# Kernel optimization log

Hardware: AMD Instinct MI355X
Metric: run time of the kernel (lower is better)

Reference implementation:

```python
import jax, jax.numpy as jnp
import numpy as np

# FARNN_S_D_W (RE2NN-SEQ), farnn=1, train_mode='sum' (real semiring -> plain matmul),
# additional_nonlinear='tanh', sigmoid_exponent=1, no CRF.
VOCAB, D, R, RW, S, C = 30000, 100, 150, 50, 50, 20
B, L = 256, 512


def setup_inputs() -> dict:
    key = jax.random.key(0)
    ks = jax.random.split(key, 18)
    f = lambda k, shp, s=0.1: (jax.random.normal(k, shp, dtype=jnp.float32) * s)
    return dict(
        tokens=jax.random.randint(ks[0], (B, L), 0, VOCAB),
        W_embed=f(ks[1], (VOCAB, D), 1.0),        # pretrained word embeddings
        embed_r=f(ks[2], (D, R)),                  # embed_r_generalized
        V_embed=f(ks[3], (VOCAB, R)),
        C_embed=f(ks[4], (C, R)),
        S1=f(ks[5], (S, R)),
        S2=f(ks[6], (S, R)),
        S1_w=f(ks[7], (S, RW)),
        S2_w=f(ks[8], (S, RW)),
        C_w=f(ks[9], (C, RW)),                     # C_wildcard
        WW=f(ks[10], (S, S)),                      # wildcard_wildcard
        h0=f(ks[11], (S,), 1.0),
        hT=f(ks[12], (S,), 1.0),
        beta_vec=jnp.full((R,), 0.5, jnp.float32),
        Wss1=f(ks[13], (S, S)),
        Wrs1=f(ks[14], (R, S)),
        bs1=jnp.full((1, S), 0.1, jnp.float32),
        prio_a=jnp.ones((C,), jnp.float32),        # PriorityLayer per-class scale
        prio_b=jnp.zeros((C,), jnp.float32),       # PriorityLayer per-class bias
    )


def reference(tokens, W_embed, embed_r, V_embed, C_embed, S1, S2, S1_w, S2_w,
              C_w, WW, h0, hT, beta_vec, Wss1, Wrs1, bs1, prio_a, prio_b):
    # precomputed class-summed vectors used for the hidden recurrence
    C_vec_sum = C_embed.sum(0)                                  # [R]
    Cw_sum = C_w.sum(0)                                         # [RW]
    # wildcard transition matrix: CP-recomposed wildcard + wildcard_wildcard
    wild_mat = jnp.einsum('sr,r,tr->st', S1_w, Cw_sum, S2_w) + WW  # [S,S]
    # readout vectors (hT contracted with S2 factors)
    u = hT @ S2                                                 # [R]
    uw = hT @ S2_w                                              # [RW]

    # generalized V embedding (blend of rule V factor and word embedding)
    emb_gen = jnp.tanh(W_embed[tokens] @ embed_r)               # [B,L,R]
    V_vec = V_embed[tokens] * beta_vec + emb_gen * (1.0 - beta_vec)  # [B,L,R]
    R_all = V_vec * C_vec_sum                                   # [B,L,R]

    h_init = jnp.broadcast_to(h0, (tokens.shape[0], h0.shape[0]))  # [B,S]

    def step(h, xs):
        v_vec, r_vec = xs                                       # [B,R] each
        # farnn==1 gate
        zt = jax.nn.sigmoid(h @ Wss1 + r_vec @ Wrs1 + bs1)      # [B,S]
        # semiring (sum) transition: CP-factored WFA step + wildcard path
        tr1 = (h @ S1) * r_vec                                  # [B,R]
        h_new = tr1 @ S2.T + h @ wild_mat                       # [B,S]
        h_next = zt * h_new + (1.0 - zt) * h
        # per-class local score at this step, then PriorityLayer affine
        sc = ((h @ S1) * v_vec * u) @ C_embed.T \
             + ((h @ S1_w) * uw) @ C_w.T                        # [B,C]
        sc = sc * prio_a + prio_b
        return h_next, sc

    xs = (jnp.swapaxes(V_vec, 0, 1), jnp.swapaxes(R_all, 0, 1))  # [L,B,R]
    _, scores = jax.lax.scan(step, h_init, xs)                   # [L,B,C]
    return jnp.swapaxes(scores, 0, 1)                            # [B,L,C]
```

## Files before the change

### kernel.cpp

```cpp
#include <hip/hip_runtime.h>
#include <hip/hip_bf16.h>

typedef __hip_bfloat16 bf16;
typedef __attribute__((ext_vector_type(8))) short short8v;
typedef __attribute__((ext_vector_type(4))) float floatx4;

#define VOCAB_ 30000
#define D_ 100
#define R_ 150
#define RW_ 50
#define S_ 50
#define C_ 20
#define B_ 256
#define L_ 512

__device__ __forceinline__ float b2f(bf16 x){ return __bfloat162float(x); }
__device__ __forceinline__ bf16  f2b(float x){ return __float2bfloat16(x); }

#define BAR() asm volatile("s_waitcnt lgkmcnt(0)\ns_barrier" ::: "memory")

__device__ __forceinline__ float qxor1(float x){
  return __int_as_float(
      __builtin_amdgcn_mov_dpp(__float_as_int(x), 0xB1, 0xF, 0xF, true));
}
__device__ __forceinline__ float qxor2(float x){
  return __int_as_float(
      __builtin_amdgcn_mov_dpp(__float_as_int(x), 0x4E, 0xF, 0xF, true));
}

__device__ __forceinline__ float ftanh(float x){
  const float e = __expf(2.f * x);
  return 1.f - 2.f * __builtin_amdgcn_rcpf(e + 1.f);
}

__device__ __forceinline__ float ldin(const void* p, long i, int isb){
  return isb ? b2f(((const bf16*)p)[i]) : ((const float*)p)[i];
}
template<int SB> __device__ __forceinline__ float4 ld4s(const void* p, long i4){
  if (SB) {
    uint2 r = *(const uint2*)((const unsigned short*)p + i4*4);
    float4 v;
    v.x = __uint_as_float((r.x & 0xffffu) << 16);
    v.y = __uint_as_float((r.x >> 16) << 16);
    v.z = __uint_as_float((r.y & 0xffffu) << 16);
    v.w = __uint_as_float((r.y >> 16) << 16);
    return v;
  } else {
    return ((const float4*)p)[i4];
  }
}

#define WS_WF   4096
#define WS_S2F  20480
#define WS_SW   28672
#define WS_HC   36864
#define WS_WT   53248
#define WS_ERB  139264
#define WS_ERBL 149504
#define WS_WRB  159744
#define WS_WRBL 164864
#define WS_HDR  786432

__global__ void k_pre1(const void* beta, const void* S2, const void* S2w,
                       const void* Ce, const void* Cw, const void* hT,
                       float* __restrict__ wsf)
{
  __shared__ float hTs[S_];
  __shared__ int sflag;
  int tid = threadIdx.x;
  if (tid == 0) {
    unsigned w = *(const unsigned*)beta;
    int f = (w == 0x3F003F00u) ? 1 : 0;
    sflag = f;
    ((int*)wsf)[3000] = f;
  }
  __syncthreads();
  const int isb = sflag;
  if (tid < S_) hTs[tid] = ldin(hT, tid, isb);
  __syncthreads();
  if (tid < R_) {
    float a = 0.f, c = 0.f;
    for (int s = 0; s < S_; ++s) a += hTs[s] * ldin(S2, s*R_ + tid, isb);
    for (int cc = 0; cc < C_; ++cc) c += ldin(Ce, cc*R_ + tid, isb);
    wsf[tid] = a;
    wsf[224 + tid] = c;
  }
  if (tid >= 192 && tid < 242) {
    int rw = tid - 192;
    float a = 0.f, c = 0.f;
    for (int s = 0; s < S_; ++s) a += hTs[s] * ldin(S2w, s*RW_ + rw, isb);
    for (int cc = 0; cc < C_; ++cc) c += ldin(Cw, cc*RW_ + rw, isb);
    wsf[160 + rw]  = a;
    wsf[2900 + rw] = c;
  }
}

__global__ void k_pre2(const void* S1, const void* S1w, const void* Wss1,
                       const void* WW, const void* S2, const void* S2w,
                       const void* Ce, const void* Cw, const void* er,
                       const void* Wrs1, float* __restrict__ wsf)
{
  const int isb = ((const int*)wsf)[3000];
  const int tid = threadIdx.x, blk = blockIdx.x;
  if (blk < 50) {
    const int s = blk;
    __shared__ float s2w[RW_*RW_];
    __shared__ float s1wc[RW_];
    for (int i = tid; i < RW_*RW_; i += 256) s2w[i] = ldin(S2w, i, isb);
    if (tid < RW_) s1wc[tid] = ldin(S1w, s*RW_ + tid, isb) * wsf[2900 + tid];
    __syncthreads();
    for (int col = tid; col < 300; col += 256) {
      float v;
      if (col < 150)       v = ldin(S1, s*R_ + col, isb);
      else if (col < 200)  v = ldin(S1w, s*RW_ + (col-150), isb);
      else if (col < 250)  v = ldin(Wss1, s*S_ + (col-200), isb);
      else {
        const int t2 = col - 250;
        float a = ldin(WW, s*S_ + t2, isb);
        for (int rw = 0; rw < RW_; ++rw) a += s1wc[rw] * s2w[t2*RW_ + rw];
        v = a;
      }
      wsf[WS_WF + col*52 + s] = v;
    }
    if (blk == 0) {
      for (int col = tid; col < 300; col += 256) {
        wsf[WS_WF + col*52 + 50] = 0.f;
        wsf[WS_WF + col*52 + 51] = 0.f;
      }
    }
    for (int r = tid; r < 160; r += 256)
      wsf[WS_S2F + s*160 + r] = (r < R_) ? ldin(S2, s*R_ + r, isb) : 0.f;
  } else if (blk < 64) {
    for (int c = blk - 50; c < C_; c += 14) {
      for (int k = tid; k < 224; k += 256) {
        float v = 0.f;
        if (k < R_)        v = ldin(Ce, c*R_ + k, isb);
        else if (k < 200)  v = wsf[160 + (k - R_)] * ldin(Cw, c*RW_ + (k - R_), isb);
        wsf[WS_SW + c*224 + k] = v;
      }
    }
  } else if (blk < 128) {
  } else if (blk < 138) {
    const int nt = blk - 128;
    bf16* ebh = (bf16*)(wsf + WS_ERB);
    bf16* ebl = (bf16*)(wsf + WS_ERBL);
    for (int i = tid; i < 2048; i += 256) {
      const int kk = i >> 9, lane = (i >> 3) & 63, j = i & 7;
      const int col = nt*16 + (lane & 15);
      const int k   = kk*32 + (lane >> 4)*8 + j;
      const float v = (col < R_ && k < D_) ? ldin(er, (long)k*R_ + col, isb) : 0.f;
      const bf16 h = f2b(v);
      ebh[((nt*4 + kk)*64 + lane)*8 + j] = h;
      ebl[((nt*4 + kk)*64 + lane)*8 + j] = f2b(v - b2f(h));
    }
  } else if (blk < 158) {
    const int idx = blk - 138, nt2 = idx / 5, kk = idx - nt2*5;
    bf16* wbh = (bf16*)(wsf + WS_WRB);
    bf16* wbl = (bf16*)(wsf + WS_WRBL);
    for (int i = tid; i < 512; i += 256) {
      const int lane = i >> 3, j = i & 7;
      const int s = nt2*16 + (lane & 15);
      const int k = kk*32 + (lane >> 4)*8 + j;
      const float v = (s < S_ && k < R_) ? ldin(Wrs1, (long)k*S_ + s, isb) : 0.f;
      const bf16 h = f2b(v);
      wbh[((nt2*5 + kk)*64 + lane)*8 + j] = h;
      wbl[((nt2*5 + kk)*64 + lane)*8 + j] = f2b(v - b2f(h));
    }
  }
}

__global__ void k_pre3(const void* pa, const void* pb, float* __restrict__ wsf)
{
  const int isb = ((const int*)wsf)[3000];
  const int tid = threadIdx.x;
  float* w = wsf + WS_WT + tid*96;
  for (int i = 0; i < 96; ++i) w[i] = 0.f;
  if (tid < 300) {
    for (int s = 0; s < 52; ++s) w[s] = wsf[WS_WF + tid*52 + s];
    if (tid < 150) { w[52] = wsf[224 + tid]; w[53] = wsf[tid]; }
    if (tid < 200) {
      const int s = tid >> 2, kc = tid & 3;
      for (int j = 0; j < 40; ++j)
        w[56 + j] = wsf[WS_S2F + s*160 + kc*40 + j];
    }
  } else if (tid >= 320 && tid < 400) {
    const int q = tid - 320, c = q >> 2, kc = q & 3;
    for (int j = 0; j < 56; ++j) w[j] = wsf[WS_SW + c*224 + kc*56 + j];
    w[56] = ldin(pa, c, isb);
    w[57] = ldin(pb, c, isb);
  }
}

__global__ __launch_bounds__(256)
void k_front_m32(const int* __restrict__ tokens, const void* Wembv,
                 const void* Vembv, const void* betav, const void* bs1v,
                 const float* __restrict__ wsf,
                 void* __restrict__ Voutv, void* __restrict__ Goutv,
                 int t0, int Lc)
{
  const float* Wemb = (const float*)Wembv;
  const float* Vemb = (const float*)Vembv;
  const float* beta = (const float*)betav;
  const float* bs1  = (const float*)bs1v;
  float* Vout = (float*)Voutv;
  float* Gout = (float*)Goutv;

  __shared__ __align__(16) char smem[49152];
  __shared__ int ldsTok[64];
  const int tid = threadIdx.x;
  const int lane = tid & 63, mt = tid >> 6;
  const int l15 = lane & 15, g = lane >> 4;
  const long rowbase = (long)blockIdx.x * 64;

  if (tid < 64) {
    long row = rowbase + tid;
    long b = row / Lc, l = row - b * Lc;
    ldsTok[tid] = tokens[b * L_ + t0 + l];
  }
  for (int i = tid; i < 640; i += 256) {
    const int row = i / 10, k = 150 + (i - (i/10)*10);
    const int off = row*384 + (((k >> 3) ^ (row & 7)) * 16) + (k & 7) * 2;
    *(unsigned short*)(smem + off) = 0;
    *(unsigned short*)(smem + 24576 + off) = 0;
  }
  __syncthreads();

  const int arow = mt*16 + l15;
  short8v afh[4], afl[4];
  {
    const float* wr = Wemb + (long)ldsTok[arow] * D_;
    #pragma unroll
    for (int kk = 0; kk < 4; ++kk) {
      const int k0 = kk*32 + g*8;
      float4 x0 = {0.f,0.f,0.f,0.f}, x1 = {0.f,0.f,0.f,0.f};
      if (k0 < D_)     x0 = *(const float4*)(wr + k0);
      if (k0 + 4 < D_) x1 = *(const float4*)(wr + k0 + 4);
      float xs[8] = {x0.x,x0.y,x0.z,x0.w,x1.x,x1.y,x1.z,x1.w};
      #pragma unroll
      for (int j = 0; j < 8; ++j) {
        const bf16 h = f2b(xs[j]);
        ((bf16*)&afh[kk])[j] = h;
        ((bf16*)&afl[kk])[j] = f2b(xs[j] - b2f(h));
      }
    }
  }

  const short8v* ebh = (const short8v*)(wsf + WS_ERB);
  const short8v* ebl = (const short8v*)(wsf + WS_ERBL);
  const floatx4 zero4 = {0.f, 0.f, 0.f, 0.f};
  floatx4 acc[10];
  #pragma unroll
  for (int nt = 0; nt < 10; ++nt) acc[nt] = zero4;
  #pragma unroll
  for (int nt = 0; nt < 10; ++nt) {
    #pragma unroll
    for (int kk = 0; kk < 4; ++kk) {
      const short8v bh = ebh[(nt*4 + kk)*64 + lane];
      const short8v bl = ebl[(nt*4 + kk)*64 + lane];
      acc[nt] = __builtin_amdgcn_mfma_f32_16x16x32_bf16(afh[kk], bh, acc[nt], 0,0,0);
      acc[nt] = __builtin_amdgcn_mfma_f32_16x16x32_bf16(afh[kk], bl, acc[nt], 0,0,0);
      acc[nt] = __builtin_amdgcn_mfma_f32_16x16x32_bf16(afl[kk], bh, acc[nt], 0,0,0);
    }
  }

  int rows[4]; long tb[4];
  #pragma unroll
  for (int i = 0; i < 4; ++i) {
    rows[i] = mt*16 + g*4 + i;
    tb[i] = (long)ldsTok[rows[i]] * R_;
  }
  #pragma unroll
  for (int nt = 0; nt < 10; ++nt) {
    const int r = nt*16 + l15;
    if (r < R_) {
      const float bet = beta[r];
      const float cs  = wsf[224 + r];
      const float ub  = 1.f - bet;
      #pragma unroll
      for (int i = 0; i < 4; ++i) {
        const float emb = ftanh(acc[nt][i]);
        const float vv  = Vemb[tb[i] + r];
        const float V   = vv * bet + emb * ub;
        Vout[(rowbase + rows[i]) * R_ + r] = V;
        const float vp = V * cs;
        const bf16 h = f2b(vp);
        const int off = rows[i]*384 + (((r >> 3) ^ (rows[i] & 7)) * 16) + (r & 7) * 2;
        *(bf16*)(smem + off) = h;
        *(bf16*)(smem + 24576 + off) = f2b(vp - b2f(h));
      }
    }
  }
  __syncthreads();

  short8v vfh[5], vfl[5];
  #pragma unroll
  for (int kk = 0; kk < 5; ++kk) {
    const int q2 = kk*4 + g;
    const int off = arow*384 + ((q2 ^ (arow & 7)) * 16);
    vfh[kk] = *(const short8v*)(smem + off);
    vfl[kk] = *(const short8v*)(smem + 24576 + off);
  }
  const short8v* wbh = (const short8v*)(wsf + WS_WRB);
  const short8v* wbl = (const short8v*)(wsf + WS_WRBL);
  floatx4 acc2[4];
  #pragma unroll
  for (int nt2 = 0; nt2 < 4; ++nt2) acc2[nt2] = zero4;
  #pragma unroll
  for (int nt2 = 0; nt2 < 4; ++nt2) {
    #pragma unroll
    for (int kk = 0; kk < 5; ++kk) {
      const short8v bh = wbh[(nt2*5 + kk)*64 + lane];
      const short8v bl = wbl[(nt2*5 + kk)*64 + lane];
      acc2[nt2] = __builtin_amdgcn_mfma_f32_16x16x32_bf16(vfh[kk], bh, acc2[nt2], 0,0,0);
      acc2[nt2] = __builtin_amdgcn_mfma_f32_16x16x32_bf16(vfh[kk], bl, acc2[nt2], 0,0,0);
      acc2[nt2] = __builtin_amdgcn_mfma_f32_16x16x32_bf16(vfl[kk], bh, acc2[nt2], 0,0,0);
    }
  }
  #pragma unroll
  for (int nt2 = 0; nt2 < 4; ++nt2) {
    const int s = nt2*16 + l15;
    if (s < S_) {
      const float bias = bs1[s];
      #pragma unroll
      for (int i = 0; i < 4; ++i)
        Gout[(rowbase + rows[i]) * S_ + s] = acc2[nt2][i] + bias;
    }
  }
}

__global__ __launch_bounds__(256)
void k_front_mfma(const int* __restrict__ tokens, const void* Wemb,
                  const void* Vemb, const void* beta, const void* bs1,
                  const float* __restrict__ wsf,
                  void* __restrict__ Vout, void* __restrict__ Gout,
                  int t0, int Lc)
{
  __shared__ __align__(16) char smem[45056];
  __shared__ int ldsTok[64];
  const int tid = threadIdx.x;
  const int lane = tid & 63, mt = tid >> 6;
  const int l15 = lane & 15, l4 = lane >> 4;
  const long rowbase = (long)blockIdx.x * 64;

  if (tid < 64) {
    long row = rowbase + tid;
    long b = row / Lc, l = row - b * Lc;
    ldsTok[tid] = tokens[b * L_ + t0 + l];
  }
  __syncthreads();

  for (int i4 = tid; i4 < 1024; i4 += 256) {
    const int row = i4 >> 4, q = i4 & 15;
    const unsigned short* wr = (const unsigned short*)Wemb + (long)ldsTok[row] * D_;
    uint2 lo = {0u, 0u}, hi = {0u, 0u};
    if (q < 12)       { lo = *(const uint2*)(wr + q*8); hi = *(const uint2*)(wr + q*8 + 4); }
    else if (q == 12) { lo = *(const uint2*)(wr + 96); }
    char* dst = smem + row*256 + ((q ^ (row & 7)) * 16);
    *(uint2*)dst = lo;
    *(uint2*)(dst + 8) = hi;
  }
  for (int i = tid; i < 1536; i += 256) {
    uint2 z = {0u, 0u};
    *(uint2*)(smem + 20480 + i*16) = z;
    *(uint2*)(smem + 20480 + i*16 + 8) = z;
  }
  __syncthreads();

  const int arow = mt*16 + l15;
  short8v af[4];
  #pragma unroll
  for (int kk = 0; kk < 4; ++kk)
    af[kk] = *(const short8v*)(smem + arow*256 + (((kk*4 + l4) ^ (arow & 7)) * 16));
  __syncthreads();

  const short8v* erb = (const short8v*)(wsf + WS_ERB);
  floatx4 zero4 = {0.f, 0.f, 0.f, 0.f};
  floatx4 acc[10];
  #pragma unroll
  for (int nt = 0; nt < 10; ++nt) acc[nt] = zero4;
  #pragma unroll
  for (int nt = 0; nt < 10; ++nt)
    #pragma unroll
    for (int kk = 0; kk < 4; ++kk)
      acc[nt] = __builtin_amdgcn_mfma_f32_16x16x32_bf16(
                    af[kk], erb[(nt*4 + kk)*64 + lane], acc[nt], 0, 0, 0);

  bf16* ldsVo = (bf16*)smem;
  int rows[4]; long tb[4];
  #pragma unroll
  for (int i = 0; i < 4; ++i) {
    rows[i] = mt*16 + l4*4 + i;
    tb[i] = (long)ldsTok[rows[i]] * R_;
  }
  const bf16* vem  = (const bf16*)Vemb;
  const bf16* betp = (const bf16*)beta;
  #pragma unroll
  for (int nt = 0; nt < 10; ++nt) {
    const int r = nt*16 + l15;
    if (r < R_) {
      const float bet = b2f(betp[r]);
      const float cs  = wsf[224 + r];
      const float ub  = 1.f - bet;
      #pragma unroll
      for (int i = 0; i < 4; ++i) {
        const float emb = ftanh(acc[nt][i]);
        const float vv  = b2f(vem[tb[i] + r]);
        const float V   = vv * bet + emb * ub;
        ldsVo[rows[i]*160 + r] = f2b(V);
        const int p = (r >> 3) ^ (rows[i] & 7);
        *(bf16*)(smem + 20480 + rows[i]*384 + p*16 + (r & 7)*2) = f2b(V * cs);
      }
    }
  }
  __syncthreads();

  short8v vf[5];
  #pragma unroll
  for (int kk = 0; kk < 5; ++kk)
    vf[kk] = *(const short8v*)(smem + 20480 + arow*384 + (((kk*4 + l4) ^ (arow & 7)) * 16));
  const short8v* wrb = (const short8v*)(wsf + WS_WRB);
  floatx4 acc2[4];
  #pragma unroll
  for (int nt2 = 0; nt2 < 4; ++nt2) acc2[nt2] = zero4;
  #pragma unroll
  for (int nt2 = 0; nt2 < 4; ++nt2)
    #pragma unroll
    for (int kk = 0; kk < 5; ++kk)
      acc2[nt2] = __builtin_amdgcn_mfma_f32_16x16x32_bf16(
                      vf[kk], wrb[(nt2*5 + kk)*64 + lane], acc2[nt2], 0, 0, 0);

  bf16* goutp = (bf16*)Gout;
  const bf16* bsp = (const bf16*)bs1;
  #pragma unroll
  for (int nt2 = 0; nt2 < 4; ++nt2) {
    const int s = nt2*16 + l15;
    if (s < S_) {
      const float bias = b2f(bsp[s]);
      #pragma unroll
      for (int i = 0; i < 4; ++i)
        goutp[(rowbase + rows[i]) * S_ + s] = f2b(acc2[nt2][i] + bias);
    }
  }
  const unsigned short* vo = (const unsigned short*)smem;
  unsigned short* vout = (unsigned short*)Vout;
  for (int i = tid; i < 4800; i += 256) {
    const int row = i / 75, q2 = i - row*75;
    const unsigned w = *(const unsigned*)(vo + row*160 + q2*2);
    *(unsigned*)(vout + (size_t)(rowbase + row)*R_ + q2*2) = w;
  }
}

template<int SB>
__global__ __launch_bounds__(448) __attribute__((amdgpu_waves_per_eu(2, 2)))
void k_rnn(const void* h0, float* __restrict__ wsf,
           const void* __restrict__ Vg, const void* __restrict__ Gg,
           void* __restrict__ out, int t0, int Lc)
{
  const int isb = ((const int*)wsf)[3000];
  float* hc = wsf + WS_HC;
  __shared__ __align__(16) float lds_h[56];
  __shared__ __align__(16) float tr1[160];
  __shared__ __align__(16) float BP[2][224];
  __shared__ float GP[52];
  __shared__ float HW[52];
  __shared__ __align__(16) float cV[2][1200];
  __shared__ __align__(16) float cG[2][400];
  __shared__ __align__(16) float scb[L_ * C_];
  const int tid = threadIdx.x;
  const int b = blockIdx.x;
  const size_t esz = SB ? 2 : 4;
  const char* Vsb = (const char*)Vg + (size_t)b * Lc * R_ * esz;
  const char* Gsb = (const char*)Gg + (size_t)b * Lc * S_ * esz;

  float4 W0,W1,W2,W3,W4,W5,W6,W7,W8,W9,W10,W11,W12,W13;
  float4 Q0,Q1,Q2,Q3,Q4,Q5,Q6,Q7,Q8,Q9;
  float2 PR;
  {
    const float4* wp = (const float4*)(wsf + WS_WT + tid*96);
    W0=wp[0]; W1=wp[1]; W2=wp[2]; W3=wp[3]; W4=wp[4];
    W5=wp[5]; W6=wp[6]; W7=wp[7]; W8=wp[8]; W9=wp[9];
    W10=wp[10]; W11=wp[11]; W12=wp[12]; W13=wp[13];
    Q0=wp[14]; Q1=wp[15]; Q2=wp[16]; Q3=wp[17]; Q4=wp[18];
    Q5=wp[19]; Q6=wp[20]; Q7=wp[21]; Q8=wp[22]; Q9=wp[23];
    PR = *(const float2*)(wsf + WS_WT + tid*96 + 56);
  }
  const int isP1 = (tid < 300);
  const int isP2 = (tid < 200);
  const int s0   = tid >> 2, kc2 = tid & 3;
  const int isSc = (tid >= 320 && tid < 400);
  const int qs   = isSc ? tid - 320 : 0;
  const int c0   = qs >> 2, kc3 = qs & 3;
  const int isPf = (tid < 400);
  const int qpf  = tid;

  float h_own = 0.f;
  if (isP2 && kc2 == 0)
    h_own = (t0 == 0) ? ldin(h0, s0, isb) : hc[(long)b*S_ + s0];

  if (tid < S_) lds_h[tid] = (t0 == 0) ? ldin(h0, tid, isb) : hc[(long)b*S_ + tid];
  else if (tid < 56) lds_h[tid] = 0.f;
  if (tid >= 64 && tid < 74) tr1[150 + (tid - 64)] = 0.f;
  if (tid >= 96 && tid < 120) { BP[0][200 + (tid-96)] = 0.f; BP[1][200 + (tid-96)] = 0.f; }

  float4 rS = {0,0,0,0};
  if (isPf) {
    #pragma unroll
    for (int ch = 0; ch < 2; ++ch) {
      float4 v = (qpf < 300) ? ld4s<SB>(Vsb, (long)ch*300 + qpf)
                             : ld4s<SB>(Gsb, (long)ch*100 + (qpf-300));
      if (qpf < 300) ((float4*)cV[ch])[qpf] = v;
      else           ((float4*)cG[ch])[qpf-300] = v;
    }
    rS = (qpf < 300) ? ld4s<SB>(Vsb, 2L*300 + qpf)
                     : ld4s<SB>(Gsb, 2L*100 + (qpf-300));
  }
  __syncthreads();

  for (int tb = 0; tb < Lc; tb += 8) {
    const int cb = (tb >> 3) & 1;
    const float* cVb = cV[cb];
    const float* cGb = cG[cb];
    #pragma unroll
    for (int cs = 0; cs < 8; ++cs) {
      if (isP1) {
        float a0=0.f, a1=0.f, a2=0.f, a3=0.f;
        const float4* h4 = (const float4*)lds_h;
#define P1Q(Wq, q) { const float4 hv = h4[q]; \
        a0 = fmaf(hv.x, Wq.x, a0); a1 = fmaf(hv.y, Wq.y, a1); \
        a2 = fmaf(hv.z, Wq.z, a2); a3 = fmaf(hv.w, Wq.w, a3); }
        P1Q(W0,0) P1Q(W1,1) P1Q(W2,2) P1Q(W3,3) P1Q(W4,4) P1Q(W5,5) P1Q(W6,6)
        P1Q(W7,7) P1Q(W8,8) P1Q(W9,9) P1Q(W10,10) P1Q(W11,11) P1Q(W12,12)
#undef P1Q
        const float a = (a0 + a1) + (a2 + a3);
        if (tid < 150) {
          const float v = cVb[cs*150 + tid];
          tr1[tid]        = a * (v * W13.x);
          BP[cs & 1][tid] = a * (v * W13.y);
        } else if (tid < 200) BP[cs & 1][tid] = a;
        else if (tid < 250)   GP[tid - 200] = a;
        else                  HW[tid - 250] = a;
      }
      if (isSc && (tb + cs > 0)) {
        const float4* bp4 = (const float4*)BP[(cs + 1) & 1] + kc3*14;
        float a0=0.f, a1=0.f, a2=0.f, a3=0.f;
#define SCQ(Wq, q) { const float4 tv = bp4[q]; \
        a0 = fmaf(tv.x, Wq.x, a0); a1 = fmaf(tv.y, Wq.y, a1); \
        a2 = fmaf(tv.z, Wq.z, a2); a3 = fmaf(tv.w, Wq.w, a3); }
        SCQ(W0,0) SCQ(W1,1) SCQ(W2,2) SCQ(W3,3) SCQ(W4,4) SCQ(W5,5) SCQ(W6,6)
        SCQ(W7,7) SCQ(W8,8) SCQ(W9,9) SCQ(W10,10) SCQ(W11,11) SCQ(W12,12) SCQ(W13,13)
#undef SCQ
        float a = (a0 + a1) + (a2 + a3);
        a += qxor1(a);
        a += qxor2(a);
        if (kc3 == 0) scb[(tb + cs - 1)*C_ + c0] = a * PR.x + PR.y;
      }
      if (cs == 0 && tb > 0 && isPf) {
        if (tb + 8 < Lc) {
          if (qpf < 300) ((float4*)cV[cb^1])[qpf] = rS;
          else           ((float4*)cG[cb^1])[qpf-300] = rS;
        }
        if (tb + 16 < Lc) {
          const long m = (tb + 16) >> 3;
          rS = (qpf < 300) ? ld4s<SB>(Vsb, m*300 + qpf)
                           : ld4s<SB>(Gsb, m*100 + (qpf-300));
        }
      }
      BAR();
      if (isP2) {
        float hw = 0.f, gp = 0.f, cg = 0.f;
        if (kc2 == 0) { hw = HW[s0]; gp = GP[s0]; cg = cGb[cs*50 + s0]; }
        const float4* tp4 = (const float4*)tr1 + kc2*10;
        float a0=0.f, a1=0.f, a2=0.f, a3=0.f;
#define TQ(Wq, q) { const float4 tv = tp4[q]; \
        a0 = fmaf(tv.x, Wq.x, a0); a1 = fmaf(tv.y, Wq.y, a1); \
        a2 = fmaf(tv.z, Wq.z, a2); a3 = fmaf(tv.w, Wq.w, a3); }
        TQ(Q0,0) TQ(Q1,1) TQ(Q2,2) TQ(Q3,3) TQ(Q4,4)
        TQ(Q5,5) TQ(Q6,6) TQ(Q7,7) TQ(Q8,8) TQ(Q9,9)
#undef TQ
        float a = (a0 + a1) + (a2 + a3);
        a += qxor1(a);
        a += qxor2(a);
        if (kc2 == 0) {
          const float hn = a + hw;
          const float x  = gp + cg;
          const float z  = 1.f / (1.f + __expf(-x));
          h_own = z * hn + (1.f - z) * h_own;
          lds_h[s0] = h_own;
        }
      }
      BAR();
    }
  }
  if (isSc) {
    const float4* bp4 = (const float4*)BP[(Lc - 1) & 1] + kc3*14;
    float a0=0.f, a1=0.f, a2=0.f, a3=0.f;
#define SCQ(Wq, q) { const float4 tv = bp4[q]; \
    a0 = fmaf(tv.x, Wq.x, a0); a1 = fmaf(tv.y, Wq.y, a1); \
    a2 = fmaf(tv.z, Wq.z, a2); a3 = fmaf(tv.w, Wq.w, a3); }
    SCQ(W0,0) SCQ(W1,1) SCQ(W2,2) SCQ(W3,3) SCQ(W4,4) SCQ(W5,5) SCQ(W6,6)
    SCQ(W7,7) SCQ(W8,8) SCQ(W9,9) SCQ(W10,10) SCQ(W11,11) SCQ(W12,12) SCQ(W13,13)
#undef SCQ
    float a = (a0 + a1) + (a2 + a3);
    a += qxor1(a);
    a += qxor2(a);
    if (kc3 == 0) scb[(Lc - 1)*C_ + c0] = a * PR.x + PR.y;
  }
  __syncthreads();
  {
    const long obase = (long)b * L_ * C_ + (long)t0 * C_;
    if (!isb) {
      float* op = (float*)out + obase;
      const int n4 = Lc * C_ / 4;
      for (int i = tid; i < n4; i += 448)
        ((float4*)op)[i] = ((const float4*)scb)[i];
    } else {
      bf16* op = (bf16*)out + obase;
      const int n = Lc * C_;
      for (int i = tid; i < n; i += 448) op[i] = f2b(scb[i]);
    }
  }
  if (tid < S_) hc[(long)b*S_ + tid] = lds_h[tid];
}

extern "C" void kernel_launch(void* const* d_in, const int* in_sizes, int n_in,
                              void* d_out, int out_size, void* d_ws, size_t ws_size,
                              hipStream_t stream) {
  const int*  tokens = (const int*) d_in[0];
  const void* Wemb   = d_in[1];
  const void* er     = d_in[2];
  const void* Vemb   = d_in[3];
  const void* Ce     = d_in[4];
  const void* S1     = d_in[5];
  const void* S2     = d_in[6];
  const void* S1w    = d_in[7];
  const void* S2w    = d_in[8];
  const void* Cw     = d_in[9];
  const void* WW     = d_in[10];
  const void* h0     = d_in[11];
  const void* hT     = d_in[12];
  const void* beta   = d_in[13];
  const void* Wss1   = d_in[14];
  const void* Wrs1   = d_in[15];
  const void* bs1    = d_in[16];
  const void* prioA  = d_in[17];
  const void* prioB  = d_in[18];
  float* wsf = (float*)d_ws;
  char* streamBase = (char*)d_ws + WS_HDR;

  const size_t hdr = WS_HDR;
  int sb = 0, Lc = L_;
  if (ws_size >= hdr + (size_t)B_*L_*200*4)       { sb = 0; Lc = L_; }
  else if (ws_size >= hdr + (size_t)B_*L_*200*2)  { sb = 1; Lc = L_; }
  else {
    sb = 0; Lc = 256;
    while (Lc >= 32 && hdr + (size_t)B_*Lc*200*4 > ws_size) Lc >>= 1;
    if (Lc < 32) {
      sb = 1; Lc = 256;
      while (Lc >= 32 && hdr + (size_t)B_*Lc*200*2 > ws_size) Lc >>= 1;
      if (Lc < 32) Lc = 32;
    }
  }
  const size_t esz = sb ? 2 : 4;
  void* Vbuf = (void*)streamBase;
  void* Gbuf = (void*)(streamBase + (size_t)B_ * Lc * R_ * esz);

  k_pre1<<<dim3(1), dim3(256), 0, stream>>>(beta, S2, S2w, Ce, Cw, hT, wsf);
  k_pre2<<<dim3(160), dim3(256), 0, stream>>>(S1, S1w, Wss1, WW, S2, S2w,
                                              Ce, Cw, er, Wrs1, wsf);
  k_pre3<<<dim3(1), dim3(448), 0, stream>>>(prioA, prioB, wsf);
  for (int t0 = 0; t0 < L_; t0 += Lc) {
    dim3 egrid(B_ * Lc / 64);
    if (sb) {
      k_front_mfma<<<egrid, dim3(256), 0, stream>>>(tokens, Wemb, Vemb, beta,
                                                    bs1, wsf, Vbuf, Gbuf, t0, Lc);
      k_rnn<1><<<dim3(B_), dim3(448), 0, stream>>>(h0, wsf, Vbuf, Gbuf, d_out, t0, Lc);
    } else {
      k_front_m32<<<egrid, dim3(256), 0, stream>>>(tokens, Wemb, Vemb, beta,
                                                   bs1, wsf, Vbuf, Gbuf, t0, Lc);
      k_rnn<0><<<dim3(B_), dim3(448), 0, stream>>>(h0, wsf, Vbuf, Gbuf, d_out, t0, Lc);
    }
  }
}
```

Measured before the change: 613.6 us.

## Merge precompute kernels and overlap front-end of second half with recurrence

Folds the three small precompute kernels into one multi-role launch, recomputing a few reductions locally so it needs no separate pass. Merges the front-end projection and the recurrence into one k_run kernel and splits the sequence into two halves with double buffers. The middle launch runs the recurrence for the first half and the front-end for the second half side by side, so the bandwidth-heavy front-end can hide behind the latency-bound scan. The cost is a more complex dispatch, double the intermediate buffers, and front blocks running at 448 threads with only 256 active.

```diff
diff --git a/kernel.cpp b/kernel.cpp
--- a/kernel.cpp
+++ b/kernel.cpp
@@ -54,60 +54,31 @@
 #define WS_S2F  20480
 #define WS_SW   28672
 #define WS_HC   36864
-#define WS_WT   53248
 #define WS_ERB  139264
 #define WS_ERBL 149504
 #define WS_WRB  159744
 #define WS_WRBL 164864
 #define WS_HDR  786432
 
-__global__ void k_pre1(const void* beta, const void* S2, const void* S2w,
-                       const void* Ce, const void* Cw, const void* hT,
-                       float* __restrict__ wsf)
+__global__ void k_pre(const void* beta, const void* S2, const void* S2w,
+                      const void* Ce, const void* Cw, const void* hT,
+                      const void* S1, const void* S1w, const void* Wss1,
+                      const void* WW, const void* er, const void* Wrs1,
+                      float* __restrict__ wsf)
 {
-  __shared__ float hTs[S_];
-  __shared__ int sflag;
-  int tid = threadIdx.x;
-  if (tid == 0) {
-    unsigned w = *(const unsigned*)beta;
-    int f = (w == 0x3F003F00u) ? 1 : 0;
-    sflag = f;
-    ((int*)wsf)[3000] = f;
-  }
-  __syncthreads();
-  const int isb = sflag;
-  if (tid < S_) hTs[tid] = ldin(hT, tid, isb);
-  __syncthreads();
-  if (tid < R_) {
-    float a = 0.f, c = 0.f;
-    for (int s = 0; s < S_; ++s) a += hTs[s] * ldin(S2, s*R_ + tid, isb);
-    for (int cc = 0; cc < C_; ++cc) c += ldin(Ce, cc*R_ + tid, isb);
-    wsf[tid] = a;
-    wsf[224 + tid] = c;
-  }
-  if (tid >= 192 && tid < 242) {
-    int rw = tid - 192;
-    float a = 0.f, c = 0.f;
-    for (int s = 0; s < S_; ++s) a += hTs[s] * ldin(S2w, s*RW_ + rw, isb);
-    for (int cc = 0; cc < C_; ++cc) c += ldin(Cw, cc*RW_ + rw, isb);
-    wsf[160 + rw]  = a;
-    wsf[2900 + rw] = c;
-  }
-}
-
-__global__ void k_pre2(const void* S1, const void* S1w, const void* Wss1,
-                       const void* WW, const void* S2, const void* S2w,
-                       const void* Ce, const void* Cw, const void* er,
-                       const void* Wrs1, float* __restrict__ wsf)
-{
-  const int isb = ((const int*)wsf)[3000];
   const int tid = threadIdx.x, blk = blockIdx.x;
+  const unsigned bw = *(const unsigned*)beta;
+  const int isb = (bw == 0x3F003F00u) ? 1 : 0;
   if (blk < 50) {
     const int s = blk;
     __shared__ float s2w[RW_*RW_];
     __shared__ float s1wc[RW_];
     for (int i = tid; i < RW_*RW_; i += 256) s2w[i] = ldin(S2w, i, isb);
-    if (tid < RW_) s1wc[tid] = ldin(S1w, s*RW_ + tid, isb) * wsf[2900 + tid];
+    if (tid < RW_) {
+      float c = 0.f;
+      for (int cc = 0; cc < C_; ++cc) c += ldin(Cw, cc*RW_ + tid, isb);
+      s1wc[tid] = ldin(S1w, s*RW_ + tid, isb) * c;
+    }
     __syncthreads();
     for (int col = tid; col < 300; col += 256) {
       float v;
@@ -131,17 +102,24 @@
     for (int r = tid; r < 160; r += 256)
       wsf[WS_S2F + s*160 + r] = (r < R_) ? ldin(S2, s*R_ + r, isb) : 0.f;
   } else if (blk < 64) {
+    __shared__ float uwsh[RW_];
+    if (tid < RW_) {
+      float a = 0.f;
+      for (int s = 0; s < S_; ++s)
+        a += ldin(hT, s, isb) * ldin(S2w, s*RW_ + tid, isb);
+      uwsh[tid] = a;
+    }
+    __syncthreads();
     for (int c = blk - 50; c < C_; c += 14) {
       for (int k = tid; k < 224; k += 256) {
         float v = 0.f;
         if (k < R_)        v = ldin(Ce, c*R_ + k, isb);
-        else if (k < 200)  v = wsf[160 + (k - R_)] * ldin(Cw, c*RW_ + (k - R_), isb);
+        else if (k < 200)  v = uwsh[k - R_] * ldin(Cw, c*RW_ + (k - R_), isb);
         wsf[WS_SW + c*224 + k] = v;
       }
     }
-  } else if (blk < 128) {
-  } else if (blk < 138) {
-    const int nt = blk - 128;
+  } else if (blk < 74) {
+    const int nt = blk - 64;
     bf16* ebh = (bf16*)(wsf + WS_ERB);
     bf16* ebl = (bf16*)(wsf + WS_ERBL);
     for (int i = tid; i < 2048; i += 256) {
@@ -153,8 +131,8 @@
       ebh[((nt*4 + kk)*64 + lane)*8 + j] = h;
       ebl[((nt*4 + kk)*64 + lane)*8 + j] = f2b(v - b2f(h));
     }
-  } else if (blk < 158) {
-    const int idx = blk - 138, nt2 = idx / 5, kk = idx - nt2*5;
+  } else if (blk < 94) {
+    const int idx = blk - 74, nt2 = idx / 5, kk = idx - nt2*5;
     bf16* wbh = (bf16*)(wsf + WS_WRB);
     bf16* wbl = (bf16*)(wsf + WS_WRBL);
     for (int i = tid; i < 512; i += 256) {
@@ -166,68 +144,57 @@
       wbh[((nt2*5 + kk)*64 + lane)*8 + j] = h;
       wbl[((nt2*5 + kk)*64 + lane)*8 + j] = f2b(v - b2f(h));
     }
-  }
-}
-
-__global__ void k_pre3(const void* pa, const void* pb, float* __restrict__ wsf)
+  } else {
+    if (tid == 0) ((int*)wsf)[3000] = isb;
+    if (tid < R_) {
+      float a = 0.f, c = 0.f;
+      for (int s = 0; s < S_; ++s) a += ldin(hT, s, isb) * ldin(S2, s*R_ + tid, isb);
+      for (int cc = 0; cc < C_; ++cc) c += ldin(Ce, cc*R_ + tid, isb);
+      wsf[tid] = a;
+      wsf[224 + tid] = c;
+    }
+  }
+}
+
+#define ARENA_SZ 49408
+
+__device__ void front_body(char* arena, int fblk, const int* __restrict__ tokens,
+                           const float* __restrict__ Wemb,
+                           const float* __restrict__ Vemb,
+                           const float* __restrict__ beta,
+                           const float* __restrict__ bs1,
+                           const float* __restrict__ wsf,
+                           float* __restrict__ Vout, float* __restrict__ Gout,
+                           int t0, int Lc)
 {
-  const int isb = ((const int*)wsf)[3000];
+  int* ldsTok = (int*)(arena + 49152);
   const int tid = threadIdx.x;
-  float* w = wsf + WS_WT + tid*96;
-  for (int i = 0; i < 96; ++i) w[i] = 0.f;
-  if (tid < 300) {
-    for (int s = 0; s < 52; ++s) w[s] = wsf[WS_WF + tid*52 + s];
-    if (tid < 150) { w[52] = wsf[224 + tid]; w[53] = wsf[tid]; }
-    if (tid < 200) {
-      const int s = tid >> 2, kc = tid & 3;
-      for (int j = 0; j < 40; ++j)
-        w[56 + j] = wsf[WS_S2F + s*160 + kc*40 + j];
-    }
-  } else if (tid >= 320 && tid < 400) {
-    const int q = tid - 320, c = q >> 2, kc = q & 3;
-    for (int j = 0; j < 56; ++j) w[j] = wsf[WS_SW + c*224 + kc*56 + j];
-    w[56] = ldin(pa, c, isb);
-    w[57] = ldin(pb, c, isb);
-  }
-}
-
-__global__ __launch_bounds__(256)
-void k_front_m32(const int* __restrict__ tokens, const void* Wembv,
-                 const void* Vembv, const void* betav, const void* bs1v,
-                 const float* __restrict__ wsf,
-                 void* __restrict__ Voutv, void* __restrict__ Goutv,
-                 int t0, int Lc)
-{
-  const float* Wemb = (const float*)Wembv;
-  const float* Vemb = (const float*)Vembv;
-  const float* beta = (const float*)betav;
-  const float* bs1  = (const float*)bs1v;
-  float* Vout = (float*)Voutv;
-  float* Gout = (float*)Goutv;
-
-  __shared__ __align__(16) char smem[49152];
-  __shared__ int ldsTok[64];
-  const int tid = threadIdx.x;
-  const int lane = tid & 63, mt = tid >> 6;
-  const int l15 = lane & 15, g = lane >> 4;
-  const long rowbase = (long)blockIdx.x * 64;
-
+  const long rowbase = (long)fblk * 64;
   if (tid < 64) {
     long row = rowbase + tid;
     long b = row / Lc, l = row - b * Lc;
     ldsTok[tid] = tokens[b * L_ + t0 + l];
   }
-  for (int i = tid; i < 640; i += 256) {
+  for (int i = tid; i < 640; i += 448) {
     const int row = i / 10, k = 150 + (i - (i/10)*10);
     const int off = row*384 + (((k >> 3) ^ (row & 7)) * 16) + (k & 7) * 2;
-    *(unsigned short*)(smem + off) = 0;
-    *(unsigned short*)(smem + 24576 + off) = 0;
+    *(unsigned short*)(arena + off) = 0;
+    *(unsigned short*)(arena + 24576 + off) = 0;
   }
   __syncthreads();
 
+  const int act = (tid < 256);
+  const int lane = tid & 63, mt = (tid >> 6) & 3;
+  const int l15 = lane & 15, g = lane >> 4;
   const int arow = mt*16 + l15;
+  const floatx4 zero4 = {0.f, 0.f, 0.f, 0.f};
+
   short8v afh[4], afl[4];
-  {
+  floatx4 acc[10];
+  #pragma unroll
+  for (int nt = 0; nt < 10; ++nt) acc[nt] = zero4;
+
+  if (act) {
     const float* wr = Wemb + (long)ldsTok[arow] * D_;
     #pragma unroll
     for (int kk = 0; kk < 4; ++kk) {
@@ -243,247 +210,108 @@
         ((bf16*)&afl[kk])[j] = f2b(xs[j] - b2f(h));
       }
     }
-  }
-
-  const short8v* ebh = (const short8v*)(wsf + WS_ERB);
-  const short8v* ebl = (const short8v*)(wsf + WS_ERBL);
-  const floatx4 zero4 = {0.f, 0.f, 0.f, 0.f};
-  floatx4 acc[10];
-  #pragma unroll
-  for (int nt = 0; nt < 10; ++nt) acc[nt] = zero4;
-  #pragma unroll
-  for (int nt = 0; nt < 10; ++nt) {
-    #pragma unroll
-    for (int kk = 0; kk < 4; ++kk) {
-      const short8v bh = ebh[(nt*4 + kk)*64 + lane];
-      const short8v bl = ebl[(nt*4 + kk)*64 + lane];
-      acc[nt] = __builtin_amdgcn_mfma_f32_16x16x32_bf16(afh[kk], bh, acc[nt], 0,0,0);
-      acc[nt] = __builtin_amdgcn_mfma_f32_16x16x32_bf16(afh[kk], bl, acc[nt], 0,0,0);
-      acc[nt] = __builtin_amdgcn_mfma_f32_16x16x32_bf16(afl[kk], bh, acc[nt], 0,0,0);
-    }
-  }
-
-  int rows[4]; long tb[4];
-  #pragma unroll
-  for (int i = 0; i < 4; ++i) {
-    rows[i] = mt*16 + g*4 + i;
-    tb[i] = (long)ldsTok[rows[i]] * R_;
-  }
-  #pragma unroll
-  for (int nt = 0; nt < 10; ++nt) {
-    const int r = nt*16 + l15;
-    if (r < R_) {
-      const float bet = beta[r];
-      const float cs  = wsf[224 + r];
-      const float ub  = 1.f - bet;
+    const short8v* ebh = (const short8v*)(wsf + WS_ERB);
+    const short8v* ebl = (const short8v*)(wsf + WS_ERBL);
+    #pragma unroll
+    for (int nt = 0; nt < 10; ++nt) {
       #pragma unroll
-      for (int i = 0; i < 4; ++i) {
-        const float emb = ftanh(acc[nt][i]);
-        const float vv  = Vemb[tb[i] + r];
-        const float V   = vv * bet + emb * ub;
-        Vout[(rowbase + rows[i]) * R_ + r] = V;
-        const float vp = V * cs;
-        const bf16 h = f2b(vp);
-        const int off = rows[i]*384 + (((r >> 3) ^ (rows[i] & 7)) * 16) + (r & 7) * 2;
-        *(bf16*)(smem + off) = h;
-        *(bf16*)(smem + 24576 + off) = f2b(vp - b2f(h));
+      for (int kk = 0; kk < 4; ++kk) {
+        const short8v bh = ebh[(nt*4 + kk)*64 + lane];
+        const short8v bl = ebl[(nt*4 + kk)*64 + lane];
+        acc[nt] = __builtin_amdgcn_mfma_f32_16x16x32_bf16(afh[kk], bh, acc[nt], 0,0,0);
+        acc[nt] = __builtin_amdgcn_mfma_f32_16x16x32_bf16(afh[kk], bl, acc[nt], 0,0,0);
+        acc[nt] = __builtin_amdgcn_mfma_f32_16x16x32_bf16(afl[kk], bh, acc[nt], 0,0,0);
+      }
+    }
+    int rows[4]; long tb[4];
+    #pragma unroll
+    for (int i = 0; i < 4; ++i) {
+      rows[i] = mt*16 + g*4 + i;
+      tb[i] = (long)ldsTok[rows[i]] * R_;
+    }
+    #pragma unroll
+    for (int nt = 0; nt < 10; ++nt) {
+      const int r = nt*16 + l15;
+      if (r < R_) {
+        const float bet = beta[r];
+        const float cs  = wsf[224 + r];
+        const float ub  = 1.f - bet;
+        #pragma unroll
+        for (int i = 0; i < 4; ++i) {
+          const float emb = ftanh(acc[nt][i]);
+          const float vv  = Vemb[tb[i] + r];
+          const float V   = vv * bet + emb * ub;
+          Vout[(rowbase + rows[i]) * R_ + r] = V;
+          const float vp = V * cs;
+          const bf16 h = f2b(vp);
+          const int off = rows[i]*384 + (((r >> 3) ^ (rows[i] & 7)) * 16) + (r & 7) * 2;
+          *(bf16*)(arena + off) = h;
+          *(bf16*)(arena + 24576 + off) = f2b(vp - b2f(h));
+        }
       }
     }
   }
   __syncthreads();
-
-  short8v vfh[5], vfl[5];
-  #pragma unroll
-  for (int kk = 0; kk < 5; ++kk) {
-    const int q2 = kk*4 + g;
-    const int off = arow*384 + ((q2 ^ (arow & 7)) * 16);
-    vfh[kk] = *(const short8v*)(smem + off);
-    vfl[kk] = *(const short8v*)(smem + 24576 + off);
-  }
-  const short8v* wbh = (const short8v*)(wsf + WS_WRB);
-  const short8v* wbl = (const short8v*)(wsf + WS_WRBL);
-  floatx4 acc2[4];
-  #pragma unroll
-  for (int nt2 = 0; nt2 < 4; ++nt2) acc2[nt2] = zero4;
-  #pragma unroll
-  for (int nt2 = 0; nt2 < 4; ++nt2) {
+  if (act) {
+    short8v vfh[5], vfl[5];
     #pragma unroll
     for (int kk = 0; kk < 5; ++kk) {
-      const short8v bh = wbh[(nt2*5 + kk)*64 + lane];
-      const short8v bl = wbl[(nt2*5 + kk)*64 + lane];
-      acc2[nt2] = __builtin_amdgcn_mfma_f32_16x16x32_bf16(vfh[kk], bh, acc2[nt2], 0,0,0);
-      acc2[nt2] = __builtin_amdgcn_mfma_f32_16x16x32_bf16(vfh[kk], bl, acc2[nt2], 0,0,0);
-      acc2[nt2] = __builtin_amdgcn_mfma_f32_16x16x32_bf16(vfl[kk], bh, acc2[nt2], 0,0,0);
-    }
-  }
-  #pragma unroll
-  for (int nt2 = 0; nt2 < 4; ++nt2) {
-    const int s = nt2*16 + l15;
-    if (s < S_) {
-      const float bias = bs1[s];
+      const int q2 = kk*4 + g;
+      const int off = arow*384 + ((q2 ^ (arow & 7)) * 16);
+      vfh[kk] = *(const short8v*)(arena + off);
+      vfl[kk] = *(const short8v*)(arena + 24576 + off);
+    }
+    const short8v* wbh = (const short8v*)(wsf + WS_WRB);
+    const short8v* wbl = (const short8v*)(wsf + WS_WRBL);
+    floatx4 acc2[4];
+    #pragma unroll
+    for (int nt2 = 0; nt2 < 4; ++nt2) acc2[nt2] = zero4;
+    #pragma unroll
+    for (int nt2 = 0; nt2 < 4; ++nt2) {
       #pragma unroll
-      for (int i = 0; i < 4; ++i)
-        Gout[(rowbase + rows[i]) * S_ + s] = acc2[nt2][i] + bias;
-    }
-  }
-}
-
-__global__ __launch_bounds__(256)
-void k_front_mfma(const int* __restrict__ tokens, const void* Wemb,
-                  const void* Vemb, const void* beta, const void* bs1,
-                  const float* __restrict__ wsf,
-                  void* __restrict__ Vout, void* __restrict__ Gout,
-                  int t0, int Lc)
-{
-  __shared__ __align__(16) char smem[45056];
-  __shared__ int ldsTok[64];
-  const int tid = threadIdx.x;
-  const int lane = tid & 63, mt = tid >> 6;
-  const int l15 = lane & 15, l4 = lane >> 4;
-  const long rowbase = (long)blockIdx.x * 64;
-
-  if (tid < 64) {
-    long row = rowbase + tid;
-    long b = row / Lc, l = row - b * Lc;
-    ldsTok[tid] = tokens[b * L_ + t0 + l];
-  }
-  __syncthreads();
-
-  for (int i4 = tid; i4 < 1024; i4 += 256) {
-    const int row = i4 >> 4, q = i4 & 15;
-    const unsigned short* wr = (const unsigned short*)Wemb + (long)ldsTok[row] * D_;
-    uint2 lo = {0u, 0u}, hi = {0u, 0u};
-    if (q < 12)       { lo = *(const uint2*)(wr + q*8); hi = *(const uint2*)(wr + q*8 + 4); }
-    else if (q == 12) { lo = *(const uint2*)(wr + 96); }
-    char* dst = smem + row*256 + ((q ^ (row & 7)) * 16);
-    *(uint2*)dst = lo;
-    *(uint2*)(dst + 8) = hi;
-  }
-  for (int i = tid; i < 1536; i += 256) {
-    uint2 z = {0u, 0u};
-    *(uint2*)(smem + 20480 + i*16) = z;
-    *(uint2*)(smem + 20480 + i*16 + 8) = z;
-  }
-  __syncthreads();
-
-  const int arow = mt*16 + l15;
-  short8v af[4];
-  #pragma unroll
-  for (int kk = 0; kk < 4; ++kk)
-    af[kk] = *(const short8v*)(smem + arow*256 + (((kk*4 + l4) ^ (arow & 7)) * 16));
-  __syncthreads();
-
-  const short8v* erb = (const short8v*)(wsf + WS_ERB);
-  floatx4 zero4 = {0.f, 0.f, 0.f, 0.f};
-  floatx4 acc[10];
-  #pragma unroll
-  for (int nt = 0; nt < 10; ++nt) acc[nt] = zero4;
-  #pragma unroll
-  for (int nt = 0; nt < 10; ++nt)
-    #pragma unroll
-    for (int kk = 0; kk < 4; ++kk)
-      acc[nt] = __builtin_amdgcn_mfma_f32_16x16x32_bf16(
-                    af[kk], erb[(nt*4 + kk)*64 + lane], acc[nt], 0, 0, 0);
-
-  bf16* ldsVo = (bf16*)smem;
-  int rows[4]; long tb[4];
-  #pragma unroll
-  for (int i = 0; i < 4; ++i) {
-    rows[i] = mt*16 + l4*4 + i;
-    tb[i] = (long)ldsTok[rows[i]] * R_;
-  }
-  const bf16* vem  = (const bf16*)Vemb;
-  const bf16* betp = (const bf16*)beta;
-  #pragma unroll
-  for (int nt = 0; nt < 10; ++nt) {
-    const int r = nt*16 + l15;
-    if (r < R_) {
-      const float bet = b2f(betp[r]);
-      const float cs  = wsf[224 + r];
-      const float ub  = 1.f - bet;
-      #pragma unroll
-      for (int i = 0; i < 4; ++i) {
-        const float emb = ftanh(acc[nt][i]);
-        const float vv  = b2f(vem[tb[i] + r]);
-        const float V   = vv * bet + emb * ub;
-        ldsVo[rows[i]*160 + r] = f2b(V);
-        const int p = (r >> 3) ^ (rows[i] & 7);
-        *(bf16*)(smem + 20480 + rows[i]*384 + p*16 + (r & 7)*2) = f2b(V * cs);
-      }
-    }
-  }
-  __syncthreads();
-
-  short8v vf[5];
-  #pragma unroll
-  for (int kk = 0; kk < 5; ++kk)
-    vf[kk] = *(const short8v*)(smem + 20480 + arow*384 + (((kk*4 + l4) ^ (arow & 7)) * 16));
-  const short8v* wrb = (const short8v*)(wsf + WS_WRB);
-  floatx4 acc2[4];
-  #pragma unroll
-  for (int nt2 = 0; nt2 < 4; ++nt2) acc2[nt2] = zero4;
-  #pragma unroll
-  for (int nt2 = 0; nt2 < 4; ++nt2)
-    #pragma unroll
-    for (int kk = 0; kk < 5; ++kk)
-      acc2[nt2] = __builtin_amdgcn_mfma_f32_16x16x32_bf16(
-                      vf[kk], wrb[(nt2*5 + kk)*64 + lane], acc2[nt2], 0, 0, 0);
-
-  bf16* goutp = (bf16*)Gout;
-  const bf16* bsp = (const bf16*)bs1;
-  #pragma unroll
-  for (int nt2 = 0; nt2 < 4; ++nt2) {
-    const int s = nt2*16 + l15;
-    if (s < S_) {
-      const float bias = b2f(bsp[s]);
-      #pragma unroll
-      for (int i = 0; i < 4; ++i)
-        goutp[(rowbase + rows[i]) * S_ + s] = f2b(acc2[nt2][i] + bias);
-    }
-  }
-  const unsigned short* vo = (const unsigned short*)smem;
-  unsigned short* vout = (unsigned short*)Vout;
-  for (int i = tid; i < 4800; i += 256) {
-    const int row = i / 75, q2 = i - row*75;
-    const unsigned w = *(const unsigned*)(vo + row*160 + q2*2);
-    *(unsigned*)(vout + (size_t)(rowbase + row)*R_ + q2*2) = w;
+      for (int kk = 0; kk < 5; ++kk) {
+        const short8v bh = wbh[(nt2*5 + kk)*64 + lane];
+        const short8v bl = wbl[(nt2*5 + kk)*64 + lane];
+        acc2[nt2] = __builtin_amdgcn_mfma_f32_16x16x32_bf16(vfh[kk], bh, acc2[nt2], 0,0,0);
+        acc2[nt2] = __builtin_amdgcn_mfma_f32_16x16x32_bf16(vfh[kk], bl, acc2[nt2], 0,0,0);
+        acc2[nt2] = __builtin_amdgcn_mfma_f32_16x16x32_bf16(vfl[kk], bh, acc2[nt2], 0,0,0);
+      }
+    }
+    #pragma unroll
+    for (int nt2 = 0; nt2 < 4; ++nt2) {
+      const int s = nt2*16 + l15;
+      if (s < S_) {
+        const float bias = bs1[s];
+        #pragma unroll
+        for (int i = 0; i < 4; ++i)
+          Gout[(rowbase + mt*16 + g*4 + i) * S_ + s] = acc2[nt2][i] + bias;
+      }
+    }
   }
 }
 
 template<int SB>
-__global__ __launch_bounds__(448) __attribute__((amdgpu_waves_per_eu(2, 2)))
-void k_rnn(const void* h0, float* __restrict__ wsf,
-           const void* __restrict__ Vg, const void* __restrict__ Gg,
-           void* __restrict__ out, int t0, int Lc)
+__device__ void rnn_body(char* arena, const void* h0, const void* pa,
+                         const void* pb, float* __restrict__ wsf,
+                         const void* __restrict__ Vg, const void* __restrict__ Gg,
+                         void* __restrict__ out, int t0, int Lc)
 {
   const int isb = ((const int*)wsf)[3000];
-  float* hc = wsf + WS_HC;
-  __shared__ __align__(16) float lds_h[56];
-  __shared__ __align__(16) float tr1[160];
-  __shared__ __align__(16) float BP[2][224];
-  __shared__ float GP[52];
-  __shared__ float HW[52];
-  __shared__ __align__(16) float cV[2][1200];
-  __shared__ __align__(16) float cG[2][400];
-  __shared__ __align__(16) float scb[L_ * C_];
+  float* hc    = wsf + WS_HC;
+  float* lds_h = (float*)arena;
+  float* tr1   = (float*)(arena + 224);
+  float* BPb   = (float*)(arena + 864);
+  float* GP    = (float*)(arena + 2656);
+  float* HW    = (float*)(arena + 2864);
+  float* cVb_  = (float*)(arena + 3072);
+  float* cGb_  = (float*)(arena + 12672);
+  float* scb   = (float*)(arena + 15872);
   const int tid = threadIdx.x;
   const int b = blockIdx.x;
   const size_t esz = SB ? 2 : 4;
   const char* Vsb = (const char*)Vg + (size_t)b * Lc * R_ * esz;
   const char* Gsb = (const char*)Gg + (size_t)b * Lc * S_ * esz;
 
-  float4 W0,W1,W2,W3,W4,W5,W6,W7,W8,W9,W10,W11,W12,W13;
-  float4 Q0,Q1,Q2,Q3,Q4,Q5,Q6,Q7,Q8,Q9;
-  float2 PR;
-  {
-    const float4* wp = (const float4*)(wsf + WS_WT + tid*96);
-    W0=wp[0]; W1=wp[1]; W2=wp[2]; W3=wp[3]; W4=wp[4];
-    W5=wp[5]; W6=wp[6]; W7=wp[7]; W8=wp[8]; W9=wp[9];
-    W10=wp[10]; W11=wp[11]; W12=wp[12]; W13=wp[13];
-    Q0=wp[14]; Q1=wp[15]; Q2=wp[16]; Q3=wp[17]; Q4=wp[18];
-    Q5=wp[19]; Q6=wp[20]; Q7=wp[21]; Q8=wp[22]; Q9=wp[23];
-    PR = *(const float2*)(wsf + WS_WT + tid*96 + 56);
-  }
   const int isP1 = (tid < 300);
   const int isP2 = (tid < 200);
   const int s0   = tid >> 2, kc2 = tid & 3;
@@ -493,6 +321,29 @@
   const int isPf = (tid < 400);
   const int qpf  = tid;
 
+  float4 Z4 = {0.f,0.f,0.f,0.f};
+  float4 W0=Z4,W1=Z4,W2=Z4,W3=Z4,W4=Z4,W5=Z4,W6=Z4,W7=Z4,W8=Z4,W9=Z4,
+         W10=Z4,W11=Z4,W12=Z4,W13=Z4;
+  float4 Q0=Z4,Q1=Z4,Q2=Z4,Q3=Z4,Q4=Z4,Q5=Z4,Q6=Z4,Q7=Z4,Q8=Z4,Q9=Z4;
+  float2 PR = {0.f, 0.f};
+  if (isP1) {
+    const float4* wf = (const float4*)(wsf + WS_WF + tid*52);
+    W0=wf[0]; W1=wf[1]; W2=wf[2]; W3=wf[3]; W4=wf[4]; W5=wf[5]; W6=wf[6];
+    W7=wf[7]; W8=wf[8]; W9=wf[9]; W10=wf[10]; W11=wf[11]; W12=wf[12];
+    if (tid < 150) { W13.x = wsf[224 + tid]; W13.y = wsf[tid]; }
+  } else if (isSc) {
+    const float4* sw = (const float4*)(wsf + WS_SW + c0*224 + kc3*56);
+    W0=sw[0]; W1=sw[1]; W2=sw[2]; W3=sw[3]; W4=sw[4]; W5=sw[5]; W6=sw[6];
+    W7=sw[7]; W8=sw[8]; W9=sw[9]; W10=sw[10]; W11=sw[11]; W12=sw[12]; W13=sw[13];
+    PR.x = ldin(pa, c0, isb);
+    PR.y = ldin(pb, c0, isb);
+  }
+  if (isP2) {
+    const float4* qf = (const float4*)(wsf + WS_S2F + s0*160 + kc2*40);
+    Q0=qf[0]; Q1=qf[1]; Q2=qf[2]; Q3=qf[3]; Q4=qf[4];
+    Q5=qf[5]; Q6=qf[6]; Q7=qf[7]; Q8=qf[8]; Q9=qf[9];
+  }
+
   float h_own = 0.f;
   if (isP2 && kc2 == 0)
     h_own = (t0 == 0) ? ldin(h0, s0, isb) : hc[(long)b*S_ + s0];
@@ -500,7 +351,7 @@
   if (tid < S_) lds_h[tid] = (t0 == 0) ? ldin(h0, tid, isb) : hc[(long)b*S_ + tid];
   else if (tid < 56) lds_h[tid] = 0.f;
   if (tid >= 64 && tid < 74) tr1[150 + (tid - 64)] = 0.f;
-  if (tid >= 96 && tid < 120) { BP[0][200 + (tid-96)] = 0.f; BP[1][200 + (tid-96)] = 0.f; }
+  if (tid >= 96 && tid < 120) { BPb[200 + (tid-96)] = 0.f; BPb[224 + 200 + (tid-96)] = 0.f; }
 
   float4 rS = {0,0,0,0};
   if (isPf) {
@@ -508,8 +359,8 @@
     for (int ch = 0; ch < 2; ++ch) {
       float4 v = (qpf < 300) ? ld4s<SB>(Vsb, (long)ch*300 + qpf)
                              : ld4s<SB>(Gsb, (long)ch*100 + (qpf-300));
-      if (qpf < 300) ((float4*)cV[ch])[qpf] = v;
-      else           ((float4*)cG[ch])[qpf-300] = v;
+      if (qpf < 300) ((float4*)(cVb_ + ch*1200))[qpf] = v;
+      else           ((float4*)(cGb_ + ch*400))[qpf-300] = v;
     }
     rS = (qpf < 300) ? ld4s<SB>(Vsb, 2L*300 + qpf)
                      : ld4s<SB>(Gsb, 2L*100 + (qpf-300));
@@ -518,8 +369,8 @@
 
   for (int tb = 0; tb < Lc; tb += 8) {
     const int cb = (tb >> 3) & 1;
-    const float* cVb = cV[cb];
-    const float* cGb = cG[cb];
+    const float* cVb = cVb_ + cb*1200;
+    const float* cGb = cGb_ + cb*400;
     #pragma unroll
     for (int cs = 0; cs < 8; ++cs) {
       if (isP1) {
@@ -534,14 +385,14 @@
         const float a = (a0 + a1) + (a2 + a3);
         if (tid < 150) {
           const float v = cVb[cs*150 + tid];
-          tr1[tid]        = a * (v * W13.x);
-          BP[cs & 1][tid] = a * (v * W13.y);
-        } else if (tid < 200) BP[cs & 1][tid] = a;
+          tr1[tid]               = a * (v * W13.x);
+          BPb[(cs & 1)*224 + tid] = a * (v * W13.y);
+        } else if (tid < 200) BPb[(cs & 1)*224 + tid] = a;
         else if (tid < 250)   GP[tid - 200] = a;
         else                  HW[tid - 250] = a;
       }
       if (isSc && (tb + cs > 0)) {
-        const float4* bp4 = (const float4*)BP[(cs + 1) & 1] + kc3*14;
+        const float4* bp4 = (const float4*)(BPb + ((cs + 1) & 1)*224) + kc3*14;
         float a0=0.f, a1=0.f, a2=0.f, a3=0.f;
 #define SCQ(Wq, q) { const float4 tv = bp4[q]; \
         a0 = fmaf(tv.x, Wq.x, a0); a1 = fmaf(tv.y, Wq.y, a1); \
@@ -556,8 +407,8 @@
       }
       if (cs == 0 && tb > 0 && isPf) {
         if (tb + 8 < Lc) {
-          if (qpf < 300) ((float4*)cV[cb^1])[qpf] = rS;
-          else           ((float4*)cG[cb^1])[qpf-300] = rS;
+          if (qpf < 300) ((float4*)(cVb_ + (cb^1)*1200))[qpf] = rS;
+          else           ((float4*)(cGb_ + (cb^1)*400))[qpf-300] = rS;
         }
         if (tb + 16 < Lc) {
           const long m = (tb + 16) >> 3;
@@ -592,7 +443,7 @@
     }
   }
   if (isSc) {
-    const float4* bp4 = (const float4*)BP[(Lc - 1) & 1] + kc3*14;
+    const float4* bp4 = (const float4*)(BPb + ((Lc - 1) & 1)*224) + kc3*14;
     float a0=0.f, a1=0.f, a2=0.f, a3=0.f;
 #define SCQ(Wq, q) { const float4 tv = bp4[q]; \
     a0 = fmaf(tv.x, Wq.x, a0); a1 = fmaf(tv.y, Wq.y, a1); \
@@ -620,6 +471,147 @@
     }
   }
   if (tid < S_) hc[(long)b*S_ + tid] = lds_h[tid];
+}
+
+template<int SB>
+__global__ __launch_bounds__(448) __attribute__((amdgpu_waves_per_eu(4, 4)))
+void k_run(const int* __restrict__ tokens, const void* Wemb, const void* Vemb,
+           const void* beta, const void* bs1, const void* h0,
+           const void* pa, const void* pb, float* __restrict__ wsf,
+           const void* Vrd, const void* Grd, void* Vwr, void* Gwr,
+           void* out, int t0r, int t0f, int Lcc, int rnnBlocks)
+{
+  __shared__ __align__(16) char arena[ARENA_SZ];
+  if ((int)blockIdx.x < rnnBlocks) {
+    rnn_body<SB>(arena, h0, pa, pb, wsf, Vrd, Grd, out, t0r, Lcc);
+  } else {
+    if (SB) return;
+    front_body(arena, (int)blockIdx.x - rnnBlocks, tokens,
+               (const float*)Wemb, (const float*)Vemb, (const float*)beta,
+               (const float*)bs1, wsf, (float*)Vwr, (float*)Gwr, t0f, Lcc);
+  }
+}
+
+__global__ __launch_bounds__(256)
+void k_front_mfma(const int* __restrict__ tokens, const void* Wemb,
+                  const void* Vemb, const void* beta, const void* bs1,
+                  const float* __restrict__ wsf,
+                  void* __restrict__ Vout, void* __restrict__ Gout,
+                  int t0, int Lc)
+{
+  __shared__ __align__(16) char smem[45056];
+  __shared__ int ldsTok[64];
+  const int tid = threadIdx.x;
+  const int lane = tid & 63, mt = tid >> 6;
+  const int l15 = lane & 15, l4 = lane >> 4;
+  const long rowbase = (long)blockIdx.x * 64;
+
+  if (tid < 64) {
+    long row = rowbase + tid;
+    long b = row / Lc, l = row - b * Lc;
+    ldsTok[tid] = tokens[b * L_ + t0 + l];
+  }
+  __syncthreads();
+
+  for (int i4 = tid; i4 < 1024; i4 += 256) {
+    const int row = i4 >> 4, q = i4 & 15;
+    const unsigned short* wr = (const unsigned short*)Wemb + (long)ldsTok[row] * D_;
+    uint2 lo = {0u, 0u}, hi = {0u, 0u};
+    if (q < 12)       { lo = *(const uint2*)(wr + q*8); hi = *(const uint2*)(wr + q*8 + 4); }
+    else if (q == 12) { lo = *(const uint2*)(wr + 96); }
+    char* dst = smem + row*256 + ((q ^ (row & 7)) * 16);
+    *(uint2*)dst = lo;
+    *(uint2*)(dst + 8) = hi;
+  }
+  for (int i = tid; i < 1536; i += 256) {
+    uint2 z = {0u, 0u};
+    *(uint2*)(smem + 20480 + i*16) = z;
+    *(uint2*)(smem + 20480 + i*16 + 8) = z;
+  }
+  __syncthreads();
+
+  const int arow = mt*16 + l15;
+  short8v af[4];
+  #pragma unroll
+  for (int kk = 0; kk < 4; ++kk)
+    af[kk] = *(const short8v*)(smem + arow*256 + (((kk*4 + l4) ^ (arow & 7)) * 16));
+  __syncthreads();
+
+  const short8v* erb = (const short8v*)(wsf + WS_ERB);
+  floatx4 zero4 = {0.f, 0.f, 0.f, 0.f};
+  floatx4 acc[10];
+  #pragma unroll
+  for (int nt = 0; nt < 10; ++nt) acc[nt] = zero4;
+  #pragma unroll
+  for (int nt = 0; nt < 10; ++nt)
+    #pragma unroll
+    for (int kk = 0; kk < 4; ++kk)
+      acc[nt] = __builtin_amdgcn_mfma_f32_16x16x32_bf16(
+                    af[kk], erb[(nt*4 + kk)*64 + lane], acc[nt], 0, 0, 0);
+
+  bf16* ldsVo = (bf16*)smem;
+  int rows[4]; long tb[4];
+  #pragma unroll
+  for (int i = 0; i < 4; ++i) {
+    rows[i] = mt*16 + l4*4 + i;
+    tb[i] = (long)ldsTok[rows[i]] * R_;
+  }
+  const bf16* vem  = (const bf16*)Vemb;
+  const bf16* betp = (const bf16*)beta;
+  #pragma unroll
+  for (int nt = 0; nt < 10; ++nt) {
+    const int r = nt*16 + l15;
+    if (r < R_) {
+      const float bet = b2f(betp[r]);
+      const float cs  = wsf[224 + r];
+      const float ub  = 1.f - bet;
+      #pragma unroll
+      for (int i = 0; i < 4; ++i) {
+        const float emb = ftanh(acc[nt][i]);
+        const float vv  = b2f(vem[tb[i] + r]);
+        const float V   = vv * bet + emb * ub;
+        ldsVo[rows[i]*160 + r] = f2b(V);
+        const int p = (r >> 3) ^ (rows[i] & 7);
+        *(bf16*)(smem + 20480 + rows[i]*384 + p*16 + (r & 7)*2) = f2b(V * cs);
+      }
+    }
+  }
+  __syncthreads();
+
+  short8v vf[5];
+  #pragma unroll
+  for (int kk = 0; kk < 5; ++kk)
+    vf[kk] = *(const short8v*)(smem + 20480 + arow*384 + (((kk*4 + l4) ^ (arow & 7)) * 16));
+  const short8v* wrb = (const short8v*)(wsf + WS_WRB);
+  floatx4 acc2[4];
+  #pragma unroll
+  for (int nt2 = 0; nt2 < 4; ++nt2) acc2[nt2] = zero4;
+  #pragma unroll
+  for (int nt2 = 0; nt2 < 4; ++nt2)
+    #pragma unroll
+    for (int kk = 0; kk < 5; ++kk)
+      acc2[nt2] = __builtin_amdgcn_mfma_f32_16x16x32_bf16(
+                      vf[kk], wrb[(nt2*5 + kk)*64 + lane], acc2[nt2], 0, 0, 0);
+
+  bf16* goutp = (bf16*)Gout;
+  const bf16* bsp = (const bf16*)bs1;
+  #pragma unroll
+  for (int nt2 = 0; nt2 < 4; ++nt2) {
+    const int s = nt2*16 + l15;
+    if (s < S_) {
+      const float bias = b2f(bsp[s]);
+      #pragma unroll
+      for (int i = 0; i < 4; ++i)
+        goutp[(rowbase + rows[i]) * S_ + s] = f2b(acc2[nt2][i] + bias);
+    }
+  }
+  const unsigned short* vo = (const unsigned short*)smem;
+  unsigned short* vout = (unsigned short*)Vout;
+  for (int i = tid; i < 4800; i += 256) {
+    const int row = i / 75, q2 = i - row*75;
+    const unsigned w = *(const unsigned*)(vo + row*160 + q2*2);
+    *(unsigned*)(vout + (size_t)(rowbase + row)*R_ + q2*2) = w;
+  }
 }
 
 extern "C" void kernel_launch(void* const* d_in, const int* in_sizes, int n_in,
@@ -645,39 +637,64 @@
   const void* prioA  = d_in[17];
   const void* prioB  = d_in[18];
   float* wsf = (float*)d_ws;
-  char* streamBase = (char*)d_ws + WS_HDR;
+  char* base = (char*)d_ws + WS_HDR;
+
+  k_pre<<<dim3(95), dim3(256), 0, stream>>>(beta, S2, S2w, Ce, Cw, hT,
+                                            S1, S1w, Wss1, WW, er, Wrs1, wsf);
 
   const size_t hdr = WS_HDR;
-  int sb = 0, Lc = L_;
-  if (ws_size >= hdr + (size_t)B_*L_*200*4)       { sb = 0; Lc = L_; }
-  else if (ws_size >= hdr + (size_t)B_*L_*200*2)  { sb = 1; Lc = L_; }
-  else {
-    sb = 0; Lc = 256;
+  if (ws_size >= hdr + (size_t)B_*L_*200*4) {
+    const int Lcc = 256;
+    const size_t vb = (size_t)B_*Lcc*R_*4, gb = (size_t)B_*Lcc*S_*4;
+    void* V0 = (void*)base;            void* G0 = (void*)(base + vb);
+    void* V1 = (void*)(base + vb + gb); void* G1 = (void*)(base + 2*vb + gb);
+    const int fgrid = B_ * Lcc / 64;
+    k_run<0><<<dim3(fgrid), dim3(448), 0, stream>>>(
+        tokens, Wemb, Vemb, beta, bs1, h0, prioA, prioB, wsf,
+        V0, G0, V0, G0, d_out, 0, 0, Lcc, 0);
+    k_run<0><<<dim3(B_ + fgrid), dim3(448), 0, stream>>>(
+        tokens, Wemb, Vemb, beta, bs1, h0, prioA, prioB, wsf,
+        V0, G0, V1, G1, d_out, 0, Lcc, Lcc, B_);
+    k_run<0><<<dim3(B_), dim3(448), 0, stream>>>(
+        tokens, Wemb, Vemb, beta, bs1, h0, prioA, prioB, wsf,
+        V1, G1, V1, G1, d_out, Lcc, 0, Lcc, B_);
+  } else if (ws_size >= hdr + (size_t)B_*L_*200*2) {
+    const int Lcc = 256;
+    const size_t vb = (size_t)B_*Lcc*R_*2;
+    void* V0 = (void*)base; void* G0 = (void*)(base + vb);
+    for (int t0 = 0; t0 < L_; t0 += Lcc) {
+      k_front_mfma<<<dim3(B_*Lcc/64), dim3(256), 0, stream>>>(
+          tokens, Wemb, Vemb, beta, bs1, wsf, V0, G0, t0, Lcc);
+      k_run<1><<<dim3(B_), dim3(448), 0, stream>>>(
+          tokens, Wemb, Vemb, beta, bs1, h0, prioA, prioB, wsf,
+          V0, G0, V0, G0, d_out, t0, 0, Lcc, B_);
+    }
+  } else {
+    int sb = 0, Lc = 256;
     while (Lc >= 32 && hdr + (size_t)B_*Lc*200*4 > ws_size) Lc >>= 1;
     if (Lc < 32) {
       sb = 1; Lc = 256;
       while (Lc >= 32 && hdr + (size_t)B_*Lc*200*2 > ws_size) Lc >>= 1;
       if (Lc < 32) Lc = 32;
     }
-  }
-  const size_t esz = sb ? 2 : 4;
-  void* Vbuf = (void*)streamBase;
-  void* Gbuf = (void*)(streamBase + (size_t)B_ * Lc * R_ * esz);
-
-  k_pre1<<<dim3(1), dim3(256), 0, stream>>>(beta, S2, S2w, Ce, Cw, hT, wsf);
-  k_pre2<<<dim3(160), dim3(256), 0, stream>>>(S1, S1w, Wss1, WW, S2, S2w,
-                                              Ce, Cw, er, Wrs1, wsf);
-  k_pre3<<<dim3(1), dim3(448), 0, stream>>>(prioA, prioB, wsf);
-  for (int t0 = 0; t0 < L_; t0 += Lc) {
-    dim3 egrid(B_ * Lc / 64);
-    if (sb) {
-      k_front_mfma<<<egrid, dim3(256), 0, stream>>>(tokens, Wemb, Vemb, beta,
-                                                    bs1, wsf, Vbuf, Gbuf, t0, Lc);
-      k_rnn<1><<<dim3(B_), dim3(448), 0, stream>>>(h0, wsf, Vbuf, Gbuf, d_out, t0, Lc);
-    } else {
-      k_front_m32<<<egrid, dim3(256), 0, stream>>>(tokens, Wemb, Vemb, beta,
-                                                   bs1, wsf, Vbuf, Gbuf, t0, Lc);
-      k_rnn<0><<<dim3(B_), dim3(448), 0, stream>>>(h0, wsf, Vbuf, Gbuf, d_out, t0, Lc);
-    }
-  }
-}
+    const size_t esz = sb ? 2 : 4;
+    void* V0 = (void*)base;
+    void* G0 = (void*)(base + (size_t)B_*Lc*R_*esz);
+    for (int t0 = 0; t0 < L_; t0 += Lc) {
+      if (sb) {
+        k_front_mfma<<<dim3(B_*Lc/64), dim3(256), 0, stream>>>(
+            tokens, Wemb, Vemb, beta, bs1, wsf, V0, G0, t0, Lc);
+        k_run<1><<<dim3(B_), dim3(448), 0, stream>>>(
+            tokens, Wemb, Vemb, beta, bs1, h0, prioA, prioB, wsf,
+            V0, G0, V0, G0, d_out, t0, 0, Lc, B_);
+      } else {
+        k_run<0><<<dim3(B_*Lc/64), dim3(448), 0, stream>>>(
+            tokens, Wemb, Vemb, beta, bs1, h0, prioA, prioB, wsf,
+            V0, G0, V0, G0, d_out, 0, t0, Lc, 0);
+        k_run<0><<<dim3(B_), dim3(448), 0, stream>>>(
+            tokens, Wemb, Vemb, beta, bs1, h0, prioA, prioB, wsf,
+            V0, G0, V0, G0, d_out, t0, 0, Lc, B_);
+      }
+    }
+  }
+}
```

Result: slower. 642.6 us (+4.7%).
